# Kernel tuning notes

Measured on AMD Instinct MI355X. Metric: run time of the kernel, lower is better.

The kernel has to match this reference:

```python
import math
import jax, jax.numpy as jnp
import numpy as np

NA = 50000   # number of query nodes
NB = 50000   # number of key/value nodes
E = 800000   # number of edges
CA = 256
CB = 256
D = 256
H = 8
DH = D // H


def setup_inputs() -> dict:
    key = jax.random.key(0)
    ks = jax.random.split(key, 8)
    s = 1.0 / math.sqrt(CA)
    return {
        "Fa": jax.random.normal(ks[0], (NA, CA), dtype=jnp.float32),
        "Fb": jax.random.normal(ks[1], (NB, CB), dtype=jnp.float32),
        "a_idx": jax.random.randint(ks[2], (E,), 0, NA, dtype=jnp.int64)
        if jax.config.jax_enable_x64 else jax.random.randint(ks[2], (E,), 0, NA, dtype=jnp.int32),
        "b_idx": jax.random.randint(ks[3], (E,), 0, NB, dtype=jnp.int64)
        if jax.config.jax_enable_x64 else jax.random.randint(ks[3], (E,), 0, NB, dtype=jnp.int32),
        # torch nn.Linear weights: (out_features, in_features), y = x @ W.T
        "Wq": jax.random.normal(ks[4], (D, CA), dtype=jnp.float32) * s,
        "Wk": jax.random.normal(ks[5], (D, CB), dtype=jnp.float32) * s,
        "Wv": jax.random.normal(ks[6], (D, CB), dtype=jnp.float32) * s,
        "Wproj": jax.random.normal(ks[7], (CA, D), dtype=jnp.float32) * s,
    }


def _edge_attention(Q, K, V, Q_idx, K_idx, n_queries):
    # Q: (Na,H,dh)  K,V: (Nb,H,dh)  Q_idx,K_idx: (E,)
    scale = 1.0 / math.sqrt(Q.shape[-1])
    logits = jnp.sum(Q[Q_idx] * K[K_idx], axis=-1) * scale      # (E, H)
    # segmented softmax over edges sharing the same query (per head)
    seg_max = jax.ops.segment_max(logits, Q_idx, num_segments=n_queries)  # (Na, H)
    seg_max = jnp.where(jnp.isfinite(seg_max), seg_max, 0.0)
    ex = jnp.exp(logits - seg_max[Q_idx])                        # (E, H)
    seg_sum = jax.ops.segment_sum(ex, Q_idx, num_segments=n_queries)      # (Na, H)
    weights = ex / jnp.maximum(seg_sum[Q_idx], 1e-30)            # (E, H)
    # scatter-add weighted values
    out = jax.ops.segment_sum(weights[..., None] * V[K_idx], Q_idx,
                              num_segments=n_queries)            # (Na, H, dh)
    return out


def reference(Fa, Fb, a_idx, b_idx, Wq, Wk, Wv, Wproj):
    Na = Fa.shape[0]
    Q = (Fa @ Wq.T).reshape(Na, H, DH)
    K = (Fb @ Wk.T).reshape(-1, H, DH)
    V = (Fb @ Wv.T).reshape(-1, H, DH)
    out = _edge_attention(Q, K, V, a_idx, b_idx, Na)
    out = out.reshape(Na, H * DH)
    return Fa + out @ Wproj.T
```

## Files before the change

kernel.cpp:

```cpp
#include <hip/hip_runtime.h>

#define DM 256
#define HEADS 8

typedef __attribute__((ext_vector_type(8))) short bf16x8;
typedef __attribute__((ext_vector_type(4))) float f32x4;
typedef __attribute__((ext_vector_type(4))) unsigned short us16x4;
typedef unsigned short us16;

__device__ __forceinline__ unsigned short f2bf(float f) {
  unsigned int u = __float_as_uint(f);
  u += 0x7fffu + ((u >> 16) & 1u);
  return (unsigned short)(u >> 16);
}
__device__ __forceinline__ float bf2f(unsigned short s) {
  return __uint_as_float(((unsigned int)s) << 16);
}

__device__ __forceinline__ void gload16(const void* g, void* l) {
  __builtin_amdgcn_global_load_lds(
      (const __attribute__((address_space(1))) void*)g,
      (__attribute__((address_space(3))) void*)l, 16, 0, 0);
}

__global__ __launch_bounds__(256) void gemm_bf16(
    const us16* __restrict__ A, const us16* __restrict__ W,
    us16* __restrict__ Cb, float* __restrict__ Cf, const float* __restrict__ R,
    int Mreal, int ldc)
{
  __shared__ us16 As[128 * 32];
  __shared__ us16 Bs[128 * 32];
  const int tid = threadIdx.x;
  const int w = tid >> 6, l = tid & 63;
  const int wr = w >> 1, wc = w & 1;
  const int rowBase = blockIdx.x * 128;
  const int colBase = blockIdx.y * 128;
  const int lr = l >> 2;
  const int lc = (l & 3) * 8;
  f32x4 acc[4][4] = {};

  for (int k0 = 0; k0 < 256; k0 += 32) {
#pragma unroll
    for (int i = 0; i < 2; ++i) {
      const int rchunk = w * 32 + i * 16;
      const int r = rchunk + lr;
      gload16(A + (size_t)(rowBase + r) * 256 + k0 + lc, &As[rchunk * 32]);
      gload16(W + (size_t)(colBase + r) * 256 + k0 + lc, &Bs[rchunk * 32]);
    }
    __syncthreads();
    bf16x8 af[4], bfr[4];
#pragma unroll
    for (int m = 0; m < 4; ++m)
      af[m] = *(const bf16x8*)&As[(wr * 64 + m * 16 + (l & 15)) * 32 + (l >> 4) * 8];
#pragma unroll
    for (int n = 0; n < 4; ++n)
      bfr[n] = *(const bf16x8*)&Bs[(wc * 64 + n * 16 + (l & 15)) * 32 + (l >> 4) * 8];
#pragma unroll
    for (int m = 0; m < 4; ++m)
#pragma unroll
      for (int n = 0; n < 4; ++n)
        acc[m][n] = __builtin_amdgcn_mfma_f32_16x16x32_bf16(af[m], bfr[n], acc[m][n], 0, 0, 0);
    __syncthreads();
  }

  const int er = (l >> 4) * 4;
  const int ec = l & 15;
#pragma unroll
  for (int m = 0; m < 4; ++m)
#pragma unroll
    for (int n = 0; n < 4; ++n)
#pragma unroll
      for (int j = 0; j < 4; ++j) {
        const int grow = rowBase + wr * 64 + m * 16 + er + j;
        const int gcol = colBase + wc * 64 + n * 16 + ec;
        const float v = acc[m][n][j];
        if (Cf) {
          if (grow < Mreal) {
            const size_t off = (size_t)grow * ldc + gcol;
            Cf[off] = v + R[off];
          }
        } else {
          Cb[(size_t)grow * ldc + gcol] = f2bf(v);
        }
      }
}

__global__ void cvt_pad(const float* __restrict__ in, us16* __restrict__ out,
                        int realRows, int padRows)
{
  const size_t idx = ((size_t)blockIdx.x * 256 + threadIdx.x) * 8;
  if (idx >= (size_t)padRows * 256) return;
  const int row = (int)(idx >> 8);
  bf16x8 o;
  if (row < realRows) {
    const float4 a = *(const float4*)(in + idx);
    const float4 b = *(const float4*)(in + idx + 4);
    o[0] = (short)f2bf(a.x); o[1] = (short)f2bf(a.y);
    o[2] = (short)f2bf(a.z); o[3] = (short)f2bf(a.w);
    o[4] = (short)f2bf(b.x); o[5] = (short)f2bf(b.y);
    o[6] = (short)f2bf(b.z); o[7] = (short)f2bf(b.w);
  } else {
    o = (bf16x8){0, 0, 0, 0, 0, 0, 0, 0};
  }
  *(bf16x8*)(out + idx) = o;
}

__global__ void cvt_wkv(const float* __restrict__ Wk, const float* __restrict__ Wv,
                        us16* __restrict__ out)
{
  const size_t idx = ((size_t)blockIdx.x * 256 + threadIdx.x) * 8;
  if (idx >= (size_t)512 * 256) return;
  const float* src = (idx < (size_t)256 * 256) ? (Wk + idx) : (Wv + idx - 256 * 256);
  const float4 a = *(const float4*)(src);
  const float4 b = *(const float4*)(src + 4);
  bf16x8 o;
  o[0] = (short)f2bf(a.x); o[1] = (short)f2bf(a.y);
  o[2] = (short)f2bf(a.z); o[3] = (short)f2bf(a.w);
  o[4] = (short)f2bf(b.x); o[5] = (short)f2bf(b.y);
  o[6] = (short)f2bf(b.z); o[7] = (short)f2bf(b.w);
  *(bf16x8*)(out + idx) = o;
}

__global__ void hist_kernel(const int* __restrict__ a_idx, int* __restrict__ counts, int E)
{
  const int e = blockIdx.x * 256 + threadIdx.x;
  if (e < E) atomicAdd(&counts[a_idx[e]], 1);
}

__global__ __launch_bounds__(256) void scan_offs(const int* __restrict__ counts,
    int* __restrict__ offs, int* __restrict__ cursor, int* __restrict__ total, int n)
{
  __shared__ int buf[256];
  __shared__ int sbase;
  const int t = threadIdx.x;
  const int i = blockIdx.x * 256 + t;
  const int v = (i < n) ? counts[i] : 0;
  buf[t] = v;
  __syncthreads();
#pragma unroll
  for (int off = 1; off < 256; off <<= 1) {
    const int x = (t >= off) ? buf[t - off] : 0;
    __syncthreads();
    buf[t] += x;
    __syncthreads();
  }
  const int incl = buf[t];
  if (t == 255) sbase = atomicAdd(total, incl);
  __syncthreads();
  if (i < n) {
    const int excl = sbase + incl - v;
    offs[i] = excl;
    cursor[i] = excl;
  }
}

__global__ void scatter_kernel(const int* __restrict__ a_idx, const int* __restrict__ b_idx,
    int* __restrict__ cursor, int* __restrict__ bel, int E)
{
  const int e = blockIdx.x * 256 + threadIdx.x;
  if (e < E) bel[atomicAdd(&cursor[a_idx[e]], 1)] = b_idx[e];
}

__global__ __launch_bounds__(256) void edge_attn(
    const us16* __restrict__ Qb, const us16* __restrict__ KVb,
    const int* __restrict__ offs, const int* __restrict__ counts,
    const int* __restrict__ bel, us16* __restrict__ outb, int NA)
{
  const int a = blockIdx.x * 4 + (threadIdx.x >> 6);
  if (a >= NA) return;
  const int l = threadIdx.x & 63;
  const float scale = 0.17677669529663687f;

  const us16x4 q4 = *(const us16x4*)(Qb + (size_t)a * 256 + l * 4);
  float q0 = bf2f(q4[0]), q1 = bf2f(q4[1]), q2 = bf2f(q4[2]), q3 = bf2f(q4[3]);

  const int start = offs[a];
  const int cnt = counts[a];
  float acc0 = 0.f, acc1 = 0.f, acc2 = 0.f, acc3 = 0.f, ssum = 0.f;

  us16x4 kc = {0, 0, 0, 0}, vc = {0, 0, 0, 0};
  if (cnt > 0) {
    const us16* kv = KVb + (size_t)bel[start] * 512;
    kc = *(const us16x4*)(kv + l * 4);
    vc = *(const us16x4*)(kv + 256 + l * 4);
  }
  for (int i = 0; i < cnt; ++i) {
    us16x4 kn = kc, vn = vc;
    if (i + 1 < cnt) {
      const us16* kv = KVb + (size_t)bel[start + i + 1] * 512;
      kn = *(const us16x4*)(kv + l * 4);
      vn = *(const us16x4*)(kv + 256 + l * 4);
    }
    float p = q0 * bf2f(kc[0]);
    p = fmaf(q1, bf2f(kc[1]), p);
    p = fmaf(q2, bf2f(kc[2]), p);
    p = fmaf(q3, bf2f(kc[3]), p);
    p += __shfl_xor(p, 1, 64);
    p += __shfl_xor(p, 2, 64);
    p += __shfl_xor(p, 4, 64);
    const float ex = __expf(p * scale);
    ssum += ex;
    acc0 = fmaf(ex, bf2f(vc[0]), acc0);
    acc1 = fmaf(ex, bf2f(vc[1]), acc1);
    acc2 = fmaf(ex, bf2f(vc[2]), acc2);
    acc3 = fmaf(ex, bf2f(vc[3]), acc3);
    kc = kn; vc = vn;
  }

  const float inv = (cnt > 0) ? 1.f / ssum : 0.f;
  us16x4 o;
  o[0] = f2bf(acc0 * inv); o[1] = f2bf(acc1 * inv);
  o[2] = f2bf(acc2 * inv); o[3] = f2bf(acc3 * inv);
  *(us16x4*)(outb + (size_t)a * 256 + l * 4) = o;
}

extern "C" void kernel_launch(void* const* d_in, const int* in_sizes, int n_in,
                              void* d_out, int out_size, void* d_ws, size_t ws_size,
                              hipStream_t stream)
{
  const float* Fa    = (const float*)d_in[0];
  const float* Fb    = (const float*)d_in[1];
  const int*   a_idx = (const int*)d_in[2];
  const int*   b_idx = (const int*)d_in[3];
  const float* Wq    = (const float*)d_in[4];
  const float* Wk    = (const float*)d_in[5];
  const float* Wv    = (const float*)d_in[6];
  const float* Wproj = (const float*)d_in[7];
  float* out = (float*)d_out;

  const int NA = in_sizes[0] / DM;
  const int NB = in_sizes[1] / DM;
  const int E  = in_sizes[2];
  const int MAp = (NA + 127) & ~127;
  const int NBp = (NB + 127) & ~127;

  us16* Fa_bf  = (us16*)d_ws;
  us16* Fb_bf  = Fa_bf  + (size_t)MAp * 256;
  us16* Qbf    = Fb_bf  + (size_t)NBp * 256;
  us16* KVbf   = Qbf    + (size_t)MAp * 256;
  us16* ATbf   = KVbf   + (size_t)NBp * 512;
  us16* Wq_bf  = ATbf   + (size_t)MAp * 256;
  us16* Wkv_bf = Wq_bf  + 256 * 256;
  us16* Wp_bf  = Wkv_bf + 512 * 256;
  int* total   = (int*)(Wp_bf + 256 * 256);
  int* counts  = total + 1;
  int* offs    = counts + NA;
  int* cursor  = offs + NA;
  int* bel     = cursor + NA;

  hipMemsetAsync(total, 0, (size_t)(NA + 1) * sizeof(int), stream);

  cvt_pad<<<MAp / 8, 256, 0, stream>>>(Fa, Fa_bf, NA, MAp);
  cvt_pad<<<NBp / 8, 256, 0, stream>>>(Fb, Fb_bf, NB, NBp);
  cvt_pad<<<32, 256, 0, stream>>>(Wq, Wq_bf, 256, 256);
  cvt_wkv<<<64, 256, 0, stream>>>(Wk, Wv, Wkv_bf);
  cvt_pad<<<32, 256, 0, stream>>>(Wproj, Wp_bf, 256, 256);

  hist_kernel<<<(E + 255) / 256, 256, 0, stream>>>(a_idx, counts, E);
  scan_offs<<<(NA + 255) / 256, 256, 0, stream>>>(counts, offs, cursor, total, NA);
  scatter_kernel<<<(E + 255) / 256, 256, 0, stream>>>(a_idx, b_idx, cursor, bel, E);

  dim3 blk(256);
  gemm_bf16<<<dim3(MAp / 128, 2), blk, 0, stream>>>(Fa_bf, Wq_bf, Qbf, nullptr, nullptr, NA, 256);
  gemm_bf16<<<dim3(NBp / 128, 4), blk, 0, stream>>>(Fb_bf, Wkv_bf, KVbf, nullptr, nullptr, NB, 512);

  edge_attn<<<(NA + 3) / 4, 256, 0, stream>>>(Qbf, KVbf, offs, counts, bel, ATbf, NA);

  gemm_bf16<<<dim3(MAp / 128, 2), blk, 0, stream>>>(ATbf, Wp_bf, nullptr, out, Fa, NA, 256);
}
```

Measured before the change: 502.5 us.

## Fuse fp32-to-bf16 input conversion into GEMMs, widen tiles, unroll edge attention

The GEMM now loads the fp32 activations directly and converts them to bf16 while staging into shared memory. This removes the separate cvt_pad passes and the bf16 copies of Fa and Fb in memory. The GEMM tile grows to 128x256 with 512 threads, and the four weight conversions merge into one kernel. The edge attention loop is unrolled by four, with four neighbours' K/V rows prefetched so more gathers are in flight. In exchange, the A tile is now loaded through registers rather than the async LDS path, and register pressure rises.

```diff
diff --git a/kernel.cpp b/kernel.cpp
--- a/kernel.cpp
+++ b/kernel.cpp
@@ -1,7 +1,6 @@
 #include <hip/hip_runtime.h>
 
 #define DM 256
-#define HEADS 8
 
 typedef __attribute__((ext_vector_type(8))) short bf16x8;
 typedef __attribute__((ext_vector_type(4))) float f32x4;
@@ -23,29 +22,47 @@
       (__attribute__((address_space(3))) void*)l, 16, 0, 0);
 }
 
-__global__ __launch_bounds__(256) void gemm_bf16(
-    const us16* __restrict__ A, const us16* __restrict__ W,
+template <bool A_FP32>
+__global__ __launch_bounds__(512) void gemm_bf16(
+    const void* __restrict__ Avoid, const us16* __restrict__ W,
     us16* __restrict__ Cb, float* __restrict__ Cf, const float* __restrict__ R,
     int Mreal, int ldc)
 {
   __shared__ us16 As[128 * 32];
-  __shared__ us16 Bs[128 * 32];
+  __shared__ us16 Bs[256 * 32];
   const int tid = threadIdx.x;
   const int w = tid >> 6, l = tid & 63;
-  const int wr = w >> 1, wc = w & 1;
+  const int wr = w >> 2, wc = w & 3;
   const int rowBase = blockIdx.x * 128;
-  const int colBase = blockIdx.y * 128;
-  const int lr = l >> 2;
-  const int lc = (l & 3) * 8;
+  const int colBase = blockIdx.y * 256;
+  const int ar = tid >> 2, ac = (tid & 3) * 8;
   f32x4 acc[4][4] = {};
 
   for (int k0 = 0; k0 < 256; k0 += 32) {
 #pragma unroll
-    for (int i = 0; i < 2; ++i) {
-      const int rchunk = w * 32 + i * 16;
-      const int r = rchunk + lr;
-      gload16(A + (size_t)(rowBase + r) * 256 + k0 + lc, &As[rchunk * 32]);
-      gload16(W + (size_t)(colBase + r) * 256 + k0 + lc, &Bs[rchunk * 32]);
+    for (int j = 0; j < 2; ++j) {
+      const int r0 = (w * 2 + j) * 16;
+      gload16(W + (size_t)(colBase + r0 + (l >> 2)) * 256 + k0 + (l & 3) * 8,
+              &Bs[r0 * 32]);
+    }
+    {
+      const int grow = rowBase + ar;
+      bf16x8 av = (bf16x8){0, 0, 0, 0, 0, 0, 0, 0};
+      if (grow < Mreal) {
+        if (A_FP32) {
+          const float* Af = (const float*)Avoid;
+          const float4 x = *(const float4*)(Af + (size_t)grow * 256 + k0 + ac);
+          const float4 y = *(const float4*)(Af + (size_t)grow * 256 + k0 + ac + 4);
+          av[0] = (short)f2bf(x.x); av[1] = (short)f2bf(x.y);
+          av[2] = (short)f2bf(x.z); av[3] = (short)f2bf(x.w);
+          av[4] = (short)f2bf(y.x); av[5] = (short)f2bf(y.y);
+          av[6] = (short)f2bf(y.z); av[7] = (short)f2bf(y.w);
+        } else {
+          const us16* Ab = (const us16*)Avoid;
+          av = *(const bf16x8*)(Ab + (size_t)grow * 256 + k0 + ac);
+        }
+      }
+      *(bf16x8*)&As[ar * 32 + ac] = av;
     }
     __syncthreads();
     bf16x8 af[4], bfr[4];
@@ -85,40 +102,23 @@
       }
 }
 
-__global__ void cvt_pad(const float* __restrict__ in, us16* __restrict__ out,
-                        int realRows, int padRows)
-{
-  const size_t idx = ((size_t)blockIdx.x * 256 + threadIdx.x) * 8;
-  if (idx >= (size_t)padRows * 256) return;
-  const int row = (int)(idx >> 8);
+__global__ void cvt_weights(const float* __restrict__ Wq, const float* __restrict__ Wk,
+                            const float* __restrict__ Wv, const float* __restrict__ Wp,
+                            us16* __restrict__ out)
+{
+  const int g = blockIdx.x * 256 + threadIdx.x;
+  const size_t e = (size_t)g * 8;
+  const int sel = (int)(e >> 16);
+  const float* src = (sel == 0) ? Wq : (sel == 1) ? Wk : (sel == 2) ? Wv : Wp;
+  const size_t loc = e & 65535;
+  const float4 x = *(const float4*)(src + loc);
+  const float4 y = *(const float4*)(src + loc + 4);
   bf16x8 o;
-  if (row < realRows) {
-    const float4 a = *(const float4*)(in + idx);
-    const float4 b = *(const float4*)(in + idx + 4);
-    o[0] = (short)f2bf(a.x); o[1] = (short)f2bf(a.y);
-    o[2] = (short)f2bf(a.z); o[3] = (short)f2bf(a.w);
-    o[4] = (short)f2bf(b.x); o[5] = (short)f2bf(b.y);
-    o[6] = (short)f2bf(b.z); o[7] = (short)f2bf(b.w);
-  } else {
-    o = (bf16x8){0, 0, 0, 0, 0, 0, 0, 0};
-  }
-  *(bf16x8*)(out + idx) = o;
-}
-
-__global__ void cvt_wkv(const float* __restrict__ Wk, const float* __restrict__ Wv,
-                        us16* __restrict__ out)
-{
-  const size_t idx = ((size_t)blockIdx.x * 256 + threadIdx.x) * 8;
-  if (idx >= (size_t)512 * 256) return;
-  const float* src = (idx < (size_t)256 * 256) ? (Wk + idx) : (Wv + idx - 256 * 256);
-  const float4 a = *(const float4*)(src);
-  const float4 b = *(const float4*)(src + 4);
-  bf16x8 o;
-  o[0] = (short)f2bf(a.x); o[1] = (short)f2bf(a.y);
-  o[2] = (short)f2bf(a.z); o[3] = (short)f2bf(a.w);
-  o[4] = (short)f2bf(b.x); o[5] = (short)f2bf(b.y);
-  o[6] = (short)f2bf(b.z); o[7] = (short)f2bf(b.w);
-  *(bf16x8*)(out + idx) = o;
+  o[0] = (short)f2bf(x.x); o[1] = (short)f2bf(x.y);
+  o[2] = (short)f2bf(x.z); o[3] = (short)f2bf(x.w);
+  o[4] = (short)f2bf(y.x); o[5] = (short)f2bf(y.y);
+  o[6] = (short)f2bf(y.z); o[7] = (short)f2bf(y.w);
+  *(bf16x8*)(out + e) = o;
 }
 
 __global__ void hist_kernel(const int* __restrict__ a_idx, int* __restrict__ counts, int E)
@@ -161,6 +161,30 @@
   if (e < E) bel[atomicAdd(&cursor[a_idx[e]], 1)] = b_idx[e];
 }
 
+#define ATTN_STEP(K, V, J)                                     \
+  if ((J) < cnt) {                                             \
+    float p = q0 * bf2f(K[0]);                                 \
+    p = fmaf(q1, bf2f(K[1]), p);                               \
+    p = fmaf(q2, bf2f(K[2]), p);                               \
+    p = fmaf(q3, bf2f(K[3]), p);                               \
+    p += __shfl_xor(p, 1, 64);                                 \
+    p += __shfl_xor(p, 2, 64);                                 \
+    p += __shfl_xor(p, 4, 64);                                 \
+    const float ex = __expf(p * scale);                        \
+    ssum += ex;                                                \
+    acc0 = fmaf(ex, bf2f(V[0]), acc0);                         \
+    acc1 = fmaf(ex, bf2f(V[1]), acc1);                         \
+    acc2 = fmaf(ex, bf2f(V[2]), acc2);                         \
+    acc3 = fmaf(ex, bf2f(V[3]), acc3);                         \
+  }
+
+#define ATTN_LOAD(K, V, IDX)                                   \
+  {                                                            \
+    const us16* kv = KVb + (size_t)bel[start + (IDX)] * 512;   \
+    K = *(const us16x4*)(kv + l * 4);                          \
+    V = *(const us16x4*)(kv + 256 + l * 4);                    \
+  }
+
 __global__ __launch_bounds__(256) void edge_attn(
     const us16* __restrict__ Qb, const us16* __restrict__ KVb,
     const int* __restrict__ offs, const int* __restrict__ counts,
@@ -172,39 +196,32 @@
   const float scale = 0.17677669529663687f;
 
   const us16x4 q4 = *(const us16x4*)(Qb + (size_t)a * 256 + l * 4);
-  float q0 = bf2f(q4[0]), q1 = bf2f(q4[1]), q2 = bf2f(q4[2]), q3 = bf2f(q4[3]);
+  const float q0 = bf2f(q4[0]), q1 = bf2f(q4[1]), q2 = bf2f(q4[2]), q3 = bf2f(q4[3]);
 
   const int start = offs[a];
   const int cnt = counts[a];
   float acc0 = 0.f, acc1 = 0.f, acc2 = 0.f, acc3 = 0.f, ssum = 0.f;
 
-  us16x4 kc = {0, 0, 0, 0}, vc = {0, 0, 0, 0};
   if (cnt > 0) {
-    const us16* kv = KVb + (size_t)bel[start] * 512;
-    kc = *(const us16x4*)(kv + l * 4);
-    vc = *(const us16x4*)(kv + 256 + l * 4);
-  }
-  for (int i = 0; i < cnt; ++i) {
-    us16x4 kn = kc, vn = vc;
-    if (i + 1 < cnt) {
-      const us16* kv = KVb + (size_t)bel[start + i + 1] * 512;
-      kn = *(const us16x4*)(kv + l * 4);
-      vn = *(const us16x4*)(kv + 256 + l * 4);
+    const int last = cnt - 1;
+    us16x4 ka, va, kb, vb, kc, vc, kd, vd;
+    ATTN_LOAD(ka, va, 0)
+    ATTN_LOAD(kb, vb, min(1, last))
+    ATTN_LOAD(kc, vc, min(2, last))
+    ATTN_LOAD(kd, vd, min(3, last))
+    for (int i = 0; i < cnt; i += 4) {
+      us16x4 na, xa, nb, xb, nc, xc, nd, xd;
+      ATTN_LOAD(na, xa, min(i + 4, last))
+      ATTN_LOAD(nb, xb, min(i + 5, last))
+      ATTN_LOAD(nc, xc, min(i + 6, last))
+      ATTN_LOAD(nd, xd, min(i + 7, last))
+      ATTN_STEP(ka, va, i + 0)
+      ATTN_STEP(kb, vb, i + 1)
+      ATTN_STEP(kc, vc, i + 2)
+      ATTN_STEP(kd, vd, i + 3)
+      ka = na; va = xa; kb = nb; vb = xb;
+      kc = nc; vc = xc; kd = nd; vd = xd;
     }
-    float p = q0 * bf2f(kc[0]);
-    p = fmaf(q1, bf2f(kc[1]), p);
-    p = fmaf(q2, bf2f(kc[2]), p);
-    p = fmaf(q3, bf2f(kc[3]), p);
-    p += __shfl_xor(p, 1, 64);
-    p += __shfl_xor(p, 2, 64);
-    p += __shfl_xor(p, 4, 64);
-    const float ex = __expf(p * scale);
-    ssum += ex;
-    acc0 = fmaf(ex, bf2f(vc[0]), acc0);
-    acc1 = fmaf(ex, bf2f(vc[1]), acc1);
-    acc2 = fmaf(ex, bf2f(vc[2]), acc2);
-    acc3 = fmaf(ex, bf2f(vc[3]), acc3);
-    kc = kn; vc = vn;
   }
 
   const float inv = (cnt > 0) ? 1.f / ssum : 0.f;
@@ -234,37 +251,28 @@
   const int MAp = (NA + 127) & ~127;
   const int NBp = (NB + 127) & ~127;
 
-  us16* Fa_bf  = (us16*)d_ws;
-  us16* Fb_bf  = Fa_bf  + (size_t)MAp * 256;
-  us16* Qbf    = Fb_bf  + (size_t)NBp * 256;
-  us16* KVbf   = Qbf    + (size_t)MAp * 256;
-  us16* ATbf   = KVbf   + (size_t)NBp * 512;
-  us16* Wq_bf  = ATbf   + (size_t)MAp * 256;
-  us16* Wkv_bf = Wq_bf  + 256 * 256;
-  us16* Wp_bf  = Wkv_bf + 512 * 256;
-  int* total   = (int*)(Wp_bf + 256 * 256);
-  int* counts  = total + 1;
-  int* offs    = counts + NA;
-  int* cursor  = offs + NA;
-  int* bel     = cursor + NA;
+  us16* Qbf   = (us16*)d_ws;
+  us16* KVbf  = Qbf   + (size_t)MAp * 256;
+  us16* ATbf  = KVbf  + (size_t)NBp * 512;
+  us16* W_all = ATbf  + (size_t)MAp * 256;
+  int* total  = (int*)(W_all + 1024 * 256);
+  int* counts = total + 1;
+  int* offs   = counts + NA;
+  int* cursor = offs + NA;
+  int* bel    = cursor + NA;
 
   hipMemsetAsync(total, 0, (size_t)(NA + 1) * sizeof(int), stream);
 
-  cvt_pad<<<MAp / 8, 256, 0, stream>>>(Fa, Fa_bf, NA, MAp);
-  cvt_pad<<<NBp / 8, 256, 0, stream>>>(Fb, Fb_bf, NB, NBp);
-  cvt_pad<<<32, 256, 0, stream>>>(Wq, Wq_bf, 256, 256);
-  cvt_wkv<<<64, 256, 0, stream>>>(Wk, Wv, Wkv_bf);
-  cvt_pad<<<32, 256, 0, stream>>>(Wproj, Wp_bf, 256, 256);
+  cvt_weights<<<128, 256, 0, stream>>>(Wq, Wk, Wv, Wproj, W_all);
 
   hist_kernel<<<(E + 255) / 256, 256, 0, stream>>>(a_idx, counts, E);
   scan_offs<<<(NA + 255) / 256, 256, 0, stream>>>(counts, offs, cursor, total, NA);
   scatter_kernel<<<(E + 255) / 256, 256, 0, stream>>>(a_idx, b_idx, cursor, bel, E);
 
-  dim3 blk(256);
-  gemm_bf16<<<dim3(MAp / 128, 2), blk, 0, stream>>>(Fa_bf, Wq_bf, Qbf, nullptr, nullptr, NA, 256);
-  gemm_bf16<<<dim3(NBp / 128, 4), blk, 0, stream>>>(Fb_bf, Wkv_bf, KVbf, nullptr, nullptr, NB, 512);
+  gemm_bf16<true><<<dim3(MAp / 128, 1), 512, 0, stream>>>(Fa, W_all, Qbf, nullptr, nullptr, NA, 256);
+  gemm_bf16<true><<<dim3(NBp / 128, 2), 512, 0, stream>>>(Fb, W_all + 256 * 256, KVbf, nullptr, nullptr, NB, 512);
 
   edge_attn<<<(NA + 3) / 4, 256, 0, stream>>>(Qbf, KVbf, offs, counts, bel, ATbf, NA);
 
-  gemm_bf16<<<dim3(MAp / 128, 2), blk, 0, stream>>>(ATbf, Wp_bf, nullptr, out, Fa, NA, 256);
-}
+  gemm_bf16<false><<<dim3(MAp / 128, 1), 512, 0, stream>>>(ATbf, W_all + 768 * 256, nullptr, out, Fa, NA, 256);
+}
```

New measurement: 437.9 us. 1.15x faster.
